# Kernel tuning notes

Measured on AMD Instinct MI355X. Metric: run time of the kernel, lower is better.

Reference implementation:

```python
import jax, jax.numpy as jnp
import numpy as np

NUM_GRAPHS = 2048      # graphs in batch
NODES_PER_GRAPH = 64   # self.num_nodes
N = NUM_GRAPHS * NODES_PER_GRAPH
D = 256                # input_scalar_dim (all-scalar irreps 256x0e)
HD_GRAPH = 64          # head_dims[0]
HD_NODE = 32           # head_dims[1]


def setup_inputs() -> dict:
    key = jax.random.key(0)
    k1, k2, k3 = jax.random.split(key, 3)
    node_features = jax.random.normal(k1, (N, D), dtype=jnp.float32)
    # sorted segment ids: 64 consecutive nodes per graph (matches unique_consecutive use)
    batch = jnp.repeat(jnp.arange(NUM_GRAPHS, dtype=jnp.int32), NODES_PER_GRAPH)
    W_graph = jax.random.normal(k2, (D, HD_GRAPH), dtype=jnp.float32) * 0.05
    b_graph = jnp.zeros((HD_GRAPH,), dtype=jnp.float32)
    W_node = jax.random.normal(k3, (D, HD_NODE), dtype=jnp.float32) * 0.05
    return {"node_features": node_features, "batch": batch,
            "W_graph": W_graph, "b_graph": b_graph, "W_node": W_node}


def reference(node_features, batch, W_graph, b_graph, W_node):
    # global_mean_pool over scalar features (here all D features are scalars)
    sums = jax.ops.segment_sum(node_features, batch, num_segments=NUM_GRAPHS)
    counts = jax.ops.segment_sum(
        jnp.ones((node_features.shape[0], 1), node_features.dtype),
        batch, num_segments=NUM_GRAPHS)
    graph_features = sums / counts                      # [G, D]
    # graph head: single branch Linear(D -> HD_GRAPH) with bias, sliced to head_dim
    graph_out = graph_features @ W_graph + b_graph      # [G, HD_GRAPH]
    # node head: LinearMLPNode 'mlp' type -> o3.Linear over scalar irreps == plain bias-free linear
    node_out = node_features @ W_node                   # [N, HD_NODE]
    return (graph_out, node_out)
```

## Files before the change

kernel.cpp:

```cpp
#include <hip/hip_runtime.h>


constexpr int NUM_GRAPHS = 2048;
constexpr int NPG = 64;
constexpr int D   = 256;
constexpr int HG  = 64;
constexpr int HN  = 32;
constexpr int KC  = 32;
constexpr int NCHUNK = D / KC;
constexpr int LSTR = 36;
constexpr int WAVES = 4;

__device__ __forceinline__ float4 wave_bfly_rows(float4 s) {
    #pragma unroll
    for (int m = 8; m <= 32; m <<= 1) {
        s.x += __shfl_xor(s.x, m, 64);
        s.y += __shfl_xor(s.y, m, 64);
        s.z += __shfl_xor(s.z, m, 64);
        s.w += __shfl_xor(s.w, m, 64);
    }
    return s;
}

__global__ __launch_bounds__(256, 4)
void fused_decoder_kernel(const float* __restrict__ nf,
                          const float* __restrict__ Wg,
                          const float* __restrict__ bg,
                          const float* __restrict__ Wn,
                          float* __restrict__ out)
{
    __shared__ float lds[WAVES][NPG * LSTR];
    __shared__ float lds_csum[WAVES][D];

    const int tid  = threadIdx.x;
    const int w    = tid >> 6;
    const int lane = tid & 63;
    const int g    = blockIdx.x * WAVES + w;

    const float* __restrict__ gbase = nf + (size_t)g * NPG * D;
    float* __restrict__ out_graph = out;
    float* __restrict__ out_node  = out + NUM_GRAPHS * HG;

    const int rbase = lane >> 3;
    const int c4    = (lane & 7) << 2;

    alignas(16) float acc[HN];
    #pragma unroll
    for (int c = 0; c < HN; ++c) acc[c] = 0.f;

    {
        float4 r[8];
        #pragma unroll
        for (int j = 0; j < 8; ++j)
            r[j] = *(const float4*)(gbase + (rbase + 8 * j) * D + c4);
        float4 s = make_float4(0.f, 0.f, 0.f, 0.f);
        #pragma unroll
        for (int j = 0; j < 8; ++j) {
            *(float4*)&lds[w][(rbase + 8 * j) * LSTR + c4] = r[j];
            s.x += r[j].x; s.y += r[j].y; s.z += r[j].z; s.w += r[j].w;
        }
        s = wave_bfly_rows(s);
        if (lane < 8) *(float4*)&lds_csum[w][c4] = s;
    }

    #pragma unroll 1
    for (int ch = 0; ch < NCHUNK; ++ch) {
        float4 r[8];
        if (ch < NCHUNK - 1) {
            #pragma unroll
            for (int j = 0; j < 8; ++j)
                r[j] = *(const float4*)(gbase + (rbase + 8 * j) * D + (ch + 1) * KC + c4);
        }

        float4 f[8];
        #pragma unroll
        for (int k4 = 0; k4 < 8; ++k4)
            f[k4] = *(const float4*)&lds[w][lane * LSTR + 4 * k4];

        if (ch < NCHUNK - 1) {
            float4 s = make_float4(0.f, 0.f, 0.f, 0.f);
            #pragma unroll
            for (int j = 0; j < 8; ++j) {
                *(float4*)&lds[w][(rbase + 8 * j) * LSTR + c4] = r[j];
                s.x += r[j].x; s.y += r[j].y; s.z += r[j].z; s.w += r[j].w;
            }
            s = wave_bfly_rows(s);
            if (lane < 8) *(float4*)&lds_csum[w][(ch + 1) * KC + c4] = s;
        }

        #pragma unroll
        for (int k4 = 0; k4 < 8; ++k4) {
            #pragma unroll
            for (int q = 0; q < 4; ++q) {
                const float fv = ((const float*)&f[k4])[q];
                const float* __restrict__ wrow = Wn + (ch * KC + k4 * 4 + q) * HN;
                #pragma unroll
                for (int cc = 0; cc < HN; ++cc)
                    acc[cc] = fmaf(fv, wrow[cc], acc[cc]);
            }
        }
    }

    #pragma unroll
    for (int j = 0; j < 8; ++j)
        *(float4*)&lds[w][lane * LSTR + 4 * j] = *(const float4*)&acc[4 * j];
    #pragma unroll
    for (int j = 0; j < 8; ++j) {
        const float4 v = *(const float4*)&lds[w][(rbase + 8 * j) * LSTR + c4];
        *(float4*)(out_node + (size_t)g * (NPG * HN) + 4 * lane + 256 * j) = v;
    }

    float accg = 0.f;
    #pragma unroll 16
    for (int k = 0; k < D; ++k)
        accg = fmaf(lds_csum[w][k], Wg[k * HG + lane], accg);
    out_graph[g * HG + lane] = accg * (1.f / 64.f) + bg[lane];
}

extern "C" void kernel_launch(void* const* d_in, const int* in_sizes, int n_in,
                              void* d_out, int out_size, void* d_ws, size_t ws_size,
                              hipStream_t stream) {
    const float* nf = (const float*)d_in[0];
    const float* Wg = (const float*)d_in[2];
    const float* bg = (const float*)d_in[3];
    const float* Wn = (const float*)d_in[4];
    float* outp = (float*)d_out;

    dim3 grid(NUM_GRAPHS / WAVES);
    dim3 block(WAVES * 64);

    hipLaunchKernelGGL(fused_decoder_kernel, grid, block, 0, stream,
                       nf, Wg, bg, Wn, outp);
}
```

Measured before the change: 263.7 us.

## Use split-bf16 MFMA for node head and split graphs across wave pairs

Replaces the scalar FMA node-head matmul with MFMA 16x16x32 bf16 instructions, using a hi/lo bf16 split (three products per tile) to keep accuracy close to fp32. Wn is converted and swizzled into LDS once per block, and each graph is now handled by two waves (32 rows each). The graph pooling and graph-head reduction are recombined through LDS. This removes the VALU-heavy FMA loop and the transposing LDS staging, at the cost of per-block weight conversion, extra conversion VALU work and block-level barriers.

```diff
diff --git a/kernel.cpp b/kernel.cpp
--- a/kernel.cpp
+++ b/kernel.cpp
@@ -8,18 +8,17 @@
 constexpr int HN  = 32;
 constexpr int KC  = 32;
 constexpr int NCHUNK = D / KC;
-constexpr int LSTR = 36;
-constexpr int WAVES = 4;
 
-__device__ __forceinline__ float4 wave_bfly_rows(float4 s) {
-    #pragma unroll
-    for (int m = 8; m <= 32; m <<= 1) {
-        s.x += __shfl_xor(s.x, m, 64);
-        s.y += __shfl_xor(s.y, m, 64);
-        s.z += __shfl_xor(s.z, m, 64);
-        s.w += __shfl_xor(s.w, m, 64);
-    }
-    return s;
+typedef short short8 __attribute__((ext_vector_type(8)));
+typedef float floatx4 __attribute__((ext_vector_type(4)));
+
+__device__ __forceinline__ short f2bf(float x) {
+    unsigned u = __float_as_uint(x);
+    unsigned r = (u + 0x7fffu + ((u >> 16) & 1u)) >> 16;
+    return (short)r;
+}
+__device__ __forceinline__ float bf2f(short h) {
+    return __uint_as_float(((unsigned)(unsigned short)h) << 16);
 }
 
 __global__ __launch_bounds__(256, 4)
@@ -29,92 +28,141 @@
                           const float* __restrict__ Wn,
                           float* __restrict__ out)
 {
-    __shared__ float lds[WAVES][NPG * LSTR];
-    __shared__ float lds_csum[WAVES][D];
+    __shared__ alignas(16) short bswz[2048 * 8];
+    __shared__ alignas(16) float csum_p[4][D];
+    __shared__ alignas(16) float gpart[4][HG];
 
     const int tid  = threadIdx.x;
     const int w    = tid >> 6;
     const int lane = tid & 63;
-    const int g    = blockIdx.x * WAVES + w;
+    const int gloc = w >> 1;
+    const int rh   = w & 1;
+    const int graph = blockIdx.x * 2 + gloc;
+    const int r15  = lane & 15;
+    const int g4   = lane >> 4;
 
-    const float* __restrict__ gbase = nf + (size_t)g * NPG * D;
+    const int row_base = graph * NPG + rh * 32;
     float* __restrict__ out_graph = out;
     float* __restrict__ out_node  = out + NUM_GRAPHS * HG;
 
-    const int rbase = lane >> 3;
-    const int c4    = (lane & 7) << 2;
+    #pragma unroll 4
+    for (int i = 0; i < 8; ++i) {
+        const int s  = tid + i * 256;
+        const int ls = s & 63, ch = (s >> 6) & 7, p = (s >> 9) & 1, n = (s >> 10) & 1;
+        const int kb = ch * KC + (ls >> 4) * 8;
+        const int c  = n * 16 + (ls & 15);
+        short8 v;
+        #pragma unroll
+        for (int e = 0; e < 8; ++e) {
+            const float x = Wn[(kb + e) * HN + c];
+            const short hi = f2bf(x);
+            v[e] = (p == 0) ? hi : f2bf(x - bf2f(hi));
+        }
+        *(short8*)&bswz[s * 8] = v;
+    }
 
-    alignas(16) float acc[HN];
+    const float* __restrict__ arow0 = nf + (size_t)(row_base + r15)      * D + g4 * 8;
+    const float* __restrict__ arow1 = nf + (size_t)(row_base + 16 + r15) * D + g4 * 8;
+    floatx4 a0lo = *(const floatx4*)(arow0);
+    floatx4 a0hi = *(const floatx4*)(arow0 + 4);
+    floatx4 a1lo = *(const floatx4*)(arow1);
+    floatx4 a1hi = *(const floatx4*)(arow1 + 4);
+
+    __syncthreads();
+
+    floatx4 acc[2][2];
     #pragma unroll
-    for (int c = 0; c < HN; ++c) acc[c] = 0.f;
-
-    {
-        float4 r[8];
+    for (int m = 0; m < 2; ++m)
         #pragma unroll
-        for (int j = 0; j < 8; ++j)
-            r[j] = *(const float4*)(gbase + (rbase + 8 * j) * D + c4);
-        float4 s = make_float4(0.f, 0.f, 0.f, 0.f);
-        #pragma unroll
-        for (int j = 0; j < 8; ++j) {
-            *(float4*)&lds[w][(rbase + 8 * j) * LSTR + c4] = r[j];
-            s.x += r[j].x; s.y += r[j].y; s.z += r[j].z; s.w += r[j].w;
-        }
-        s = wave_bfly_rows(s);
-        if (lane < 8) *(float4*)&lds_csum[w][c4] = s;
-    }
+        for (int n = 0; n < 2; ++n)
+            acc[m][n] = (floatx4){0.f, 0.f, 0.f, 0.f};
 
     #pragma unroll 1
     for (int ch = 0; ch < NCHUNK; ++ch) {
-        float4 r[8];
-        if (ch < NCHUNK - 1) {
-            #pragma unroll
-            for (int j = 0; j < 8; ++j)
-                r[j] = *(const float4*)(gbase + (rbase + 8 * j) * D + (ch + 1) * KC + c4);
+        float a[2][8];
+        #pragma unroll
+        for (int e = 0; e < 4; ++e) {
+            a[0][e] = a0lo[e]; a[0][4 + e] = a0hi[e];
+            a[1][e] = a1lo[e]; a[1][4 + e] = a1hi[e];
         }
 
-        float4 f[8];
+        if (ch < NCHUNK - 1) {
+            const int ko = (ch + 1) * KC;
+            a0lo = *(const floatx4*)(arow0 + ko);
+            a0hi = *(const floatx4*)(arow0 + ko + 4);
+            a1lo = *(const floatx4*)(arow1 + ko);
+            a1hi = *(const floatx4*)(arow1 + ko + 4);
+        }
+
+        float s8[8];
         #pragma unroll
-        for (int k4 = 0; k4 < 8; ++k4)
-            f[k4] = *(const float4*)&lds[w][lane * LSTR + 4 * k4];
+        for (int e = 0; e < 8; ++e) s8[e] = a[0][e] + a[1][e];
+        #pragma unroll
+        for (int m = 1; m <= 8; m <<= 1) {
+            #pragma unroll
+            for (int e = 0; e < 8; ++e) s8[e] += __shfl_xor(s8[e], m, 64);
+        }
+        if (r15 == 0) {
+            float* cp = &csum_p[w][ch * KC + g4 * 8];
+            *(floatx4*)cp       = (floatx4){s8[0], s8[1], s8[2], s8[3]};
+            *(floatx4*)(cp + 4) = (floatx4){s8[4], s8[5], s8[6], s8[7]};
+        }
 
-        if (ch < NCHUNK - 1) {
-            float4 s = make_float4(0.f, 0.f, 0.f, 0.f);
+        short8 ahi[2], alo[2];
+        #pragma unroll
+        for (int m = 0; m < 2; ++m) {
             #pragma unroll
-            for (int j = 0; j < 8; ++j) {
-                *(float4*)&lds[w][(rbase + 8 * j) * LSTR + c4] = r[j];
-                s.x += r[j].x; s.y += r[j].y; s.z += r[j].z; s.w += r[j].w;
+            for (int e = 0; e < 8; ++e) {
+                const short h = f2bf(a[m][e]);
+                ahi[m][e] = h;
+                alo[m][e] = f2bf(a[m][e] - bf2f(h));
             }
-            s = wave_bfly_rows(s);
-            if (lane < 8) *(float4*)&lds_csum[w][(ch + 1) * KC + c4] = s;
+        }
+
+        short8 bhi[2], blo[2];
+        #pragma unroll
+        for (int n = 0; n < 2; ++n) {
+            bhi[n] = *(const short8*)&bswz[(((n * 2 + 0) * 8 + ch) * 64 + lane) * 8];
+            blo[n] = *(const short8*)&bswz[(((n * 2 + 1) * 8 + ch) * 64 + lane) * 8];
         }
 
         #pragma unroll
-        for (int k4 = 0; k4 < 8; ++k4) {
+        for (int m = 0; m < 2; ++m)
             #pragma unroll
-            for (int q = 0; q < 4; ++q) {
-                const float fv = ((const float*)&f[k4])[q];
-                const float* __restrict__ wrow = Wn + (ch * KC + k4 * 4 + q) * HN;
-                #pragma unroll
-                for (int cc = 0; cc < HN; ++cc)
-                    acc[cc] = fmaf(fv, wrow[cc], acc[cc]);
+            for (int n = 0; n < 2; ++n) {
+                acc[m][n] = __builtin_amdgcn_mfma_f32_16x16x32_bf16(ahi[m], bhi[n], acc[m][n], 0, 0, 0);
+                acc[m][n] = __builtin_amdgcn_mfma_f32_16x16x32_bf16(ahi[m], blo[n], acc[m][n], 0, 0, 0);
+                acc[m][n] = __builtin_amdgcn_mfma_f32_16x16x32_bf16(alo[m], bhi[n], acc[m][n], 0, 0, 0);
             }
-        }
     }
 
     #pragma unroll
-    for (int j = 0; j < 8; ++j)
-        *(float4*)&lds[w][lane * LSTR + 4 * j] = *(const float4*)&acc[4 * j];
-    #pragma unroll
-    for (int j = 0; j < 8; ++j) {
-        const float4 v = *(const float4*)&lds[w][(rbase + 8 * j) * LSTR + c4];
-        *(float4*)(out_node + (size_t)g * (NPG * HN) + 4 * lane + 256 * j) = v;
+    for (int m = 0; m < 2; ++m)
+        #pragma unroll
+        for (int n = 0; n < 2; ++n)
+            #pragma unroll
+            for (int r = 0; r < 4; ++r)
+                out_node[(size_t)(row_base + 16 * m + g4 * 4 + r) * HN + 16 * n + r15]
+                    = acc[m][n][r];
+
+    __syncthreads();
+    {
+        const float* cp0 = csum_p[2 * gloc];
+        const float* cp1 = csum_p[2 * gloc + 1];
+        const int k0 = rh * 128;
+        float accg = 0.f;
+        #pragma unroll 16
+        for (int k = 0; k < 128; ++k) {
+            const float cs = cp0[k0 + k] + cp1[k0 + k];
+            accg = fmaf(cs, Wg[(k0 + k) * HG + lane], accg);
+        }
+        gpart[w][lane] = accg;
     }
-
-    float accg = 0.f;
-    #pragma unroll 16
-    for (int k = 0; k < D; ++k)
-        accg = fmaf(lds_csum[w][k], Wg[k * HG + lane], accg);
-    out_graph[g * HG + lane] = accg * (1.f / 64.f) + bg[lane];
+    __syncthreads();
+    if (rh == 0) {
+        const float v = (gpart[w][lane] + gpart[w + 1][lane]) * (1.f / 64.f) + bg[lane];
+        out_graph[graph * HG + lane] = v;
+    }
 }
 
 extern "C" void kernel_launch(void* const* d_in, const int* in_sizes, int n_in,
@@ -126,8 +174,8 @@
     const float* Wn = (const float*)d_in[4];
     float* outp = (float*)d_out;
 
-    dim3 grid(NUM_GRAPHS / WAVES);
-    dim3 block(WAVES * 64);
+    dim3 grid(NUM_GRAPHS / 2);
+    dim3 block(256);
 
     hipLaunchKernelGGL(fused_decoder_kernel, grid, block, 0, stream,
                        nf, Wg, bg, Wn, outp);
```

Result: faster. 218.8 us (-17.0%).
